# Performance work log

Measured on AMD Instinct MI355X. Metric: run time of the kernel, lower is better.

Reference implementation:

```python
import jax, jax.numpy as jnp
import numpy as np

H = 512  # hidden_dim
IN = 4   # input_dim
OUT = 2  # output_dim
T_OBS = 30
T_PRED = 60
B = 4096


def _gru_cell(x, h, Wih, Whh, bih, bhh):
    # PyTorch GRU cell math. x: (B, D_in), h: (B, H)
    gi = x @ Wih.T + bih          # (B, 3H)
    gh = h @ Whh.T + bhh          # (B, 3H)
    i_r, i_z, i_n = jnp.split(gi, 3, axis=-1)
    h_r, h_z, h_n = jnp.split(gh, 3, axis=-1)
    r = jax.nn.sigmoid(i_r + h_r)
    z = jax.nn.sigmoid(i_z + h_z)
    n = jnp.tanh(i_n + r * h_n)
    return (1.0 - z) * n + z * h


def _gru_layer(xs, h0, Wih, Whh, bih, bhh):
    # xs: (T, B, D_in) -> outputs (T, B, H), final h (B, H)
    def step(h, x):
        h_new = _gru_cell(x, h, Wih, Whh, bih, bhh)
        return h_new, h_new
    h_last, ys = jax.lax.scan(step, h0, xs)
    return ys, h_last


def setup_inputs() -> dict:
    key = jax.random.key(0)
    ks = jax.random.split(key, 16)
    s = 0.05
    inp = {
        "x": jax.random.normal(ks[0], (B, T_OBS, IN), dtype=jnp.float32),
        # encoder layer 0
        "W_ih0": jax.random.normal(ks[1], (3 * H, IN)) * s,
        "W_hh0": jax.random.normal(ks[2], (3 * H, H)) * s,
        "b_ih0": jax.random.normal(ks[3], (3 * H,)) * s,
        "b_hh0": jax.random.normal(ks[4], (3 * H,)) * s,
        # encoder layer 1
        "W_ih1": jax.random.normal(ks[5], (3 * H, H)) * s,
        "W_hh1": jax.random.normal(ks[6], (3 * H, H)) * s,
        "b_ih1": jax.random.normal(ks[7], (3 * H,)) * s,
        "b_hh1": jax.random.normal(ks[8], (3 * H,)) * s,
        # decoder GRU (input_dim = OUT)
        "W_ihd": jax.random.normal(ks[9], (3 * H, OUT)) * s,
        "W_hhd": jax.random.normal(ks[10], (3 * H, H)) * s,
        "b_ihd": jax.random.normal(ks[11], (3 * H,)) * s,
        "b_hhd": jax.random.normal(ks[12], (3 * H,)) * s,
        # output head
        "W_fc": jax.random.normal(ks[13], (OUT, H)) * s,
        "b_fc": jax.random.normal(ks[14], (OUT,)) * s,
    }
    return inp


def reference(x, W_ih0, W_hh0, b_ih0, b_hh0, W_ih1, W_hh1, b_ih1, b_hh1,
              W_ihd, W_hhd, b_ihd, b_hhd, W_fc, b_fc):
    dtype = x.dtype
    xs = jnp.transpose(x, (1, 0, 2))  # (T, B, IN)
    h0 = jnp.zeros((x.shape[0], H), dtype=dtype)
    # 2-layer encoder GRU (dropout=identity at inference)
    ys0, _ = _gru_layer(xs, h0, W_ih0, W_hh0, b_ih0, b_hh0)
    ys1, h_last = _gru_layer(ys0, h0, W_ih1, W_hh1, b_ih1, b_hh1)
    dec_in0 = x[:, -1, :2]  # (B, 2)

    def dec_step(carry, _):
        h, inp = carry
        h_new = _gru_cell(inp, h, W_ihd, W_hhd, b_ihd, b_hhd)
        pred = h_new @ W_fc.T + b_fc  # (B, 2)
        return (h_new, pred), pred

    (_, _), preds = jax.lax.scan(dec_step, (h_last, dec_in0), None, length=T_PRED)
    return jnp.transpose(preds, (1, 0, 2))  # (B, T_PRED, OUT)
```

## Files before the change

### kernel.cpp

```cpp
#include <hip/hip_runtime.h>
#include <math.h>


#define B_SZ  4096
#define H     512
#define H3    1536
#define TOBS  30
#define TPRED 60

typedef float f32x4 __attribute__((ext_vector_type(4)));
typedef short s16x8 __attribute__((ext_vector_type(8)));
typedef __bf16 bf16x8 __attribute__((ext_vector_type(8)));

__device__ __forceinline__ float b2f(unsigned short u) {
    unsigned v = (unsigned)u << 16; return __builtin_bit_cast(float, v);
}
__device__ __forceinline__ unsigned short f2b(float f) {
    unsigned u = __builtin_bit_cast(unsigned, f);
    return (unsigned short)((u + 0x7FFF + ((u >> 16) & 1)) >> 16);
}

typedef __attribute__((address_space(1))) void gvoid;
typedef __attribute__((address_space(3))) void lvoid;
__device__ __forceinline__ void gl16(const void* g, void* l) {
    __builtin_amdgcn_global_load_lds((gvoid*)g, (lvoid*)l, 16, 0, 0);
}

__device__ __forceinline__ f32x4 mfma_bf16(s16x8 a, s16x8 b, f32x4 c) {
    return __builtin_amdgcn_mfma_f32_16x16x32_bf16(
        __builtin_bit_cast(bf16x8, a), __builtin_bit_cast(bf16x8, b), c, 0, 0, 0);
}

__device__ __forceinline__ float sigmoidf_(float v) { return 1.f / (1.f + expf(-v)); }

template<int NJ, int KTOT>
__device__ __forceinline__ void gemm_core2(
    const unsigned short* __restrict__ A, const unsigned short* __restrict__ W,
    int m0, int n0,
    unsigned short* __restrict__ sA, unsigned short* __restrict__ sB,
    f32x4 (&acc)[4][NJ])
{
    const int tid  = threadIdx.x;
    const int lane = tid & 63;
    const int w    = tid >> 6;
    const int wr = w >> 1, wc = w & 1;
    const int lr = lane & 15;
    const int q  = lane >> 4;
    const int wbase = tid & ~63;
    const int NT = KTOT / 64;
    const int ASZ = 128 * 64, BSZ = NJ * 32 * 64;

    auto stage = [&](int buf, int k0) {
        unsigned short* dA = sA + buf * ASZ;
        unsigned short* dB = sB + buf * BSZ;
#pragma unroll
        for (int s = 0; s < 4; ++s) {
            int i = s * 256 + tid;
            int row = i >> 3, p = i & 7;
            int c = p ^ (row & 7);
            gl16(A + (size_t)(m0 + row) * 1024 + k0 + c * 8, dA + (s * 256 + wbase) * 8);
        }
#pragma unroll
        for (int s = 0; s < NJ; ++s) {
            int i = s * 256 + tid;
            int row = i >> 3, p = i & 7;
            int c = p ^ (row & 7);
            gl16(W + (size_t)(n0 + row) * KTOT + k0 + c * 8, dB + (s * 256 + wbase) * 8);
        }
    };

    stage(0, 0);
    __syncthreads();
#pragma unroll
    for (int ti = 0; ti < NT; ++ti) {
        const int cur = ti & 1;
        if (ti + 1 < NT) stage(cur ^ 1, (ti + 1) * 64);
        const unsigned short* cA = sA + cur * ASZ;
        const unsigned short* cB = sB + cur * BSZ;
#pragma unroll
        for (int kk = 0; kk < 64; kk += 32) {
            int qb = (kk >> 3) + q;
            s16x8 af[4], bf[NJ];
#pragma unroll
            for (int fi = 0; fi < 4; ++fi) {
                int r = wr * 64 + fi * 16 + lr;
                af[fi] = *(const s16x8*)&cA[r * 64 + ((qb ^ (r & 7)) * 8)];
            }
#pragma unroll
            for (int fj = 0; fj < NJ; ++fj) {
                int r = wc * (NJ * 16) + fj * 16 + lr;
                bf[fj] = *(const s16x8*)&cB[r * 64 + ((qb ^ (r & 7)) * 8)];
            }
#pragma unroll
            for (int fi = 0; fi < 4; ++fi)
#pragma unroll
                for (int fj = 0; fj < NJ; ++fj)
                    acc[fi][fj] = mfma_bf16(af[fi], bf[fj], acc[fi][fj]);
        }
        __syncthreads();
    }
}

__global__ __launch_bounds__(256)
void gemm_e0(const unsigned short* __restrict__ A, const unsigned short* __restrict__ W,
             const float* __restrict__ x, int t,
             const float* __restrict__ Wih, const float* __restrict__ bih,
             const float* __restrict__ bhh,
             float* __restrict__ hf, unsigned short* __restrict__ hbout)
{
    int bid = (int)blockIdx.x;
    int swz = (bid & 7) * 64 + (bid >> 3);
    const int tile_n = swz & 15;
    const int n0 = tile_n * 96;
    const int m0 = (swz >> 4) * 128;

    __shared__ unsigned short sA[2 * 128 * 64], sB[2 * 96 * 64];
    f32x4 acc[4][3];
#pragma unroll
    for (int i = 0; i < 4; ++i)
#pragma unroll
        for (int j = 0; j < 3; ++j) acc[i][j] = (f32x4){0.f, 0.f, 0.f, 0.f};

    gemm_core2<3, 512>(A, W, m0, n0, sA, sB, acc);

    const int lane = threadIdx.x & 63;
    const int w    = threadIdx.x >> 6;
    const int wrw = w >> 1, wcw = w & 1;
    const int lr = lane & 15, q = lane >> 4;
    const int u = tile_n * 32 + wcw * 16 + lr;

    float4 wrv = *(const float4*)(Wih + (size_t)u * 4);
    float4 wzv = *(const float4*)(Wih + (size_t)(512 + u) * 4);
    float4 wnv = *(const float4*)(Wih + (size_t)(1024 + u) * 4);
    float br_ = bih[u], bz_ = bih[512 + u], bn_ = bih[1024 + u];
    float cr_ = bhh[u], cz_ = bhh[512 + u], cn_ = bhh[1024 + u];

#pragma unroll
    for (int fi = 0; fi < 4; ++fi) {
#pragma unroll
        for (int j = 0; j < 4; ++j) {
            int row = m0 + wrw * 64 + fi * 16 + q * 4 + j;
            float4 xv = *(const float4*)(x + (size_t)row * 120 + t * 4);
            float gir = br_ + xv.x * wrv.x + xv.y * wrv.y + xv.z * wrv.z + xv.w * wrv.w;
            float giz = bz_ + xv.x * wzv.x + xv.y * wzv.y + xv.z * wzv.z + xv.w * wzv.w;
            float gin = bn_ + xv.x * wnv.x + xv.y * wnv.y + xv.z * wnv.z + xv.w * wnv.w;
            float rr = sigmoidf_(gir + acc[fi][0][j] + cr_);
            float zz = sigmoidf_(giz + acc[fi][1][j] + cz_);
            float nn = tanhf(gin + rr * (acc[fi][2][j] + cn_));
            size_t hidx = (size_t)row * 512 + u;
            float hn = (1.f - zz) * nn + zz * hf[hidx];
            hf[hidx] = hn;
            hbout[(size_t)row * 1024 + u] = f2b(hn);
        }
    }
}

__global__ __launch_bounds__(256)
void gemm_e1(const unsigned short* __restrict__ A, const unsigned short* __restrict__ W,
             const float* __restrict__ bih, const float* __restrict__ bhh,
             float* __restrict__ hf, unsigned short* __restrict__ hbout )
{
    int bid = (int)blockIdx.x;
    int swz = (bid & 7) * 64 + (bid >> 3);
    const int tile_n = swz & 15;
    const int n0 = tile_n * 128;
    const int m0 = (swz >> 4) * 128;

    __shared__ unsigned short sA[2 * 128 * 64], sB[2 * 128 * 64];
    f32x4 acc[4][4];
#pragma unroll
    for (int i = 0; i < 4; ++i)
#pragma unroll
        for (int j = 0; j < 4; ++j) acc[i][j] = (f32x4){0.f, 0.f, 0.f, 0.f};

    gemm_core2<4, 1024>(A, W, m0, n0, sA, sB, acc);

    const int lane = threadIdx.x & 63;
    const int w    = threadIdx.x >> 6;
    const int wrw = w >> 1, wcw = w & 1;
    const int lr = lane & 15, q = lane >> 4;
    const int u = tile_n * 32 + wcw * 16 + lr;

    float br_ = bih[u] + bhh[u];
    float bz_ = bih[512 + u] + bhh[512 + u];
    float bni = bih[1024 + u], bnh = bhh[1024 + u];

#pragma unroll
    for (int fi = 0; fi < 4; ++fi) {
#pragma unroll
        for (int j = 0; j < 4; ++j) {
            int row = m0 + wrw * 64 + fi * 16 + q * 4 + j;
            float rr = sigmoidf_(acc[fi][0][j] + br_);
            float zz = sigmoidf_(acc[fi][1][j] + bz_);
            float nn = tanhf(acc[fi][2][j] + bni + rr * (acc[fi][3][j] + bnh));
            size_t hidx = (size_t)row * 512 + u;
            float hn = (1.f - zz) * nn + zz * hf[hidx];
            hf[hidx] = hn;
            hbout[(size_t)row * 1024 + u] = f2b(hn);
        }
    }
}

__global__ __launch_bounds__(256)
void gemm_d(const unsigned short* __restrict__ A ,
            const unsigned short* __restrict__ W,
            const float* __restrict__ dinbuf, int t,
            const float* __restrict__ Wih, const float* __restrict__ bih,
            const float* __restrict__ bhh, const float* __restrict__ bfc,
            float* __restrict__ hf, unsigned short* __restrict__ hbout ,
            float* __restrict__ out)
{
    int bid = (int)blockIdx.x;
    int swz = (bid & 7) * 64 + (bid >> 3);
    const int tile_n = swz & 15;
    const int n0 = tile_n * 128;
    const int m0 = (swz >> 4) * 128;

    __shared__ unsigned short sA[2 * 128 * 64], sB[2 * 128 * 64];
    f32x4 acc[4][4];
#pragma unroll
    for (int i = 0; i < 4; ++i)
#pragma unroll
        for (int j = 0; j < 4; ++j) acc[i][j] = (f32x4){0.f, 0.f, 0.f, 0.f};

    gemm_core2<4, 512>(A, W, m0, n0, sA, sB, acc);

    const int lane = threadIdx.x & 63;
    const int w    = threadIdx.x >> 6;
    const int wrw = w >> 1, wcw = w & 1;
    const int lr = lane & 15, q = lane >> 4;
    const int u = tile_n * 32 + wcw * 16 + lr;

    float wr0 = Wih[(size_t)u * 2],          wr1 = Wih[(size_t)u * 2 + 1];
    float wz0 = Wih[(size_t)(512 + u) * 2],  wz1 = Wih[(size_t)(512 + u) * 2 + 1];
    float wn0 = Wih[(size_t)(1024 + u) * 2], wn1 = Wih[(size_t)(1024 + u) * 2 + 1];
    float br_ = bih[u], bz_ = bih[512 + u], bn_ = bih[1024 + u];
    float cr_ = bhh[u], cz_ = bhh[512 + u], cn_ = bhh[1024 + u];
    float bfc0 = bfc[0], bfc1 = bfc[1];
    const bool wout = (tile_n == 0) && (wcw == 0) && (lr == 0);

#pragma unroll
    for (int fi = 0; fi < 4; ++fi) {
#pragma unroll
        for (int j = 0; j < 4; ++j) {
            int row = m0 + wrw * 64 + fi * 16 + q * 4 + j;
            float p0 = __shfl(acc[fi][3][j], (lane & 48) | 0) + bfc0;
            float p1 = __shfl(acc[fi][3][j], (lane & 48) | 1) + bfc1;
            float x0, x1;
            if (t == 0) { x0 = dinbuf[row * 2]; x1 = dinbuf[row * 2 + 1]; }
            else        { x0 = p0; x1 = p1; }
            float gir = br_ + x0 * wr0 + x1 * wr1;
            float giz = bz_ + x0 * wz0 + x1 * wz1;
            float gin = bn_ + x0 * wn0 + x1 * wn1;
            float rr = sigmoidf_(gir + acc[fi][0][j] + cr_);
            float zz = sigmoidf_(giz + acc[fi][1][j] + cz_);
            float nn = tanhf(gin + rr * (acc[fi][2][j] + cn_));
            size_t hidx = (size_t)row * 512 + u;
            float hn = (1.f - zz) * nn + zz * hf[hidx];
            hf[hidx] = hn;
            hbout[(size_t)row * 1024 + u] = f2b(hn);
            if (t > 0 && wout) {
                out[(size_t)row * 120 + (t - 1) * 2 + 0] = p0;
                out[(size_t)row * 120 + (t - 1) * 2 + 1] = p1;
            }
        }
    }
}

__global__ __launch_bounds__(64)
void fc_last(const unsigned short* __restrict__ hb ,
             const float* __restrict__ Wfc, const float* __restrict__ bfc,
             float* __restrict__ out)
{
    int row = blockIdx.x, lane = threadIdx.x;
    const unsigned short* hrow = hb + (size_t)row * 1024;
    float a0 = 0.f, a1 = 0.f;
#pragma unroll
    for (int kb = 0; kb < 8; ++kb) {
        int k = kb * 64 + lane;
        float hv = b2f(hrow[k]);
        a0 += hv * Wfc[k];
        a1 += hv * Wfc[512 + k];
    }
#pragma unroll
    for (int m = 32; m; m >>= 1) { a0 += __shfl_xor(a0, m); a1 += __shfl_xor(a1, m); }
    if (lane == 0) {
        out[(size_t)row * 120 + 118] = a0 + bfc[0];
        out[(size_t)row * 120 + 119] = a1 + bfc[1];
    }
}

__global__ void wprep_rzn(const float* __restrict__ s, unsigned short* __restrict__ d)
{
    int i = blockIdx.x * 256 + threadIdx.x;
    int c = i >> 9, k = i & 511;
    int ublock = c / 48, rem = c % 48, g = rem >> 4, uoff = rem & 15;
    int u = ublock * 16 + uoff;
    d[i] = f2b(s[((size_t)(g * 512 + u)) * 512 + k]);
}

__global__ void wprep_e1(const float* __restrict__ Wih1, const float* __restrict__ Whh1,
                         unsigned short* __restrict__ d)
{
    int i = blockIdx.x * 256 + threadIdx.x;
    int c = i >> 10, k = i & 1023;
    int ublock = c >> 6, g = (c >> 4) & 3, uoff = c & 15;
    int u = ublock * 16 + uoff;
    float v;
    if (g == 0)      v = (k < 512) ? Wih1[(size_t)u * 512 + k]          : Whh1[(size_t)u * 512 + (k - 512)];
    else if (g == 1) v = (k < 512) ? Wih1[(size_t)(512 + u) * 512 + k]  : Whh1[(size_t)(512 + u) * 512 + (k - 512)];
    else if (g == 2) v = (k < 512) ? Wih1[(size_t)(1024 + u) * 512 + k] : 0.f;
    else             v = (k < 512) ? 0.f : Whh1[(size_t)(1024 + u) * 512 + (k - 512)];
    d[i] = f2b(v);
}

__global__ void wprep_d(const float* __restrict__ Whhd, const float* __restrict__ Wfc,
                        unsigned short* __restrict__ d)
{
    int i = blockIdx.x * 256 + threadIdx.x;
    int c = i >> 9, k = i & 511;
    int ublock = c >> 6, g = (c >> 4) & 3, uoff = c & 15;
    int u = ublock * 16 + uoff;
    float v;
    if (g < 3)           v = Whhd[((size_t)(g * 512 + u)) * 512 + k];
    else if (uoff < 2)   v = Wfc[(size_t)uoff * 512 + k];
    else                 v = 0.f;
    d[i] = f2b(v);
}

__global__ void init_all(const float* __restrict__ x,
                         float* __restrict__ hf0, float* __restrict__ hf1,
                         unsigned short* __restrict__ hbU, unsigned short* __restrict__ hbV,
                         float* __restrict__ dinbuf)
{
    int idx = blockIdx.x * 256 + threadIdx.x;
    if (idx < B_SZ * 512) { hf0[idx] = 0.f; hf1[idx] = 0.f; }
    hbU[idx] = 0; hbV[idx] = 0;
    if (idx < B_SZ * 2)
        dinbuf[idx] = x[(size_t)(idx >> 1) * 120 + 29 * 4 + (idx & 1)];
}

extern "C" void kernel_launch(void* const* d_in, const int* in_sizes, int n_in,
                              void* d_out, int out_size, void* d_ws, size_t ws_size,
                              hipStream_t stream)
{
    const float* x    = (const float*)d_in[0];
    const float* Wih0 = (const float*)d_in[1];
    const float* Whh0 = (const float*)d_in[2];
    const float* bih0 = (const float*)d_in[3];
    const float* bhh0 = (const float*)d_in[4];
    const float* Wih1 = (const float*)d_in[5];
    const float* Whh1 = (const float*)d_in[6];
    const float* bih1 = (const float*)d_in[7];
    const float* bhh1 = (const float*)d_in[8];
    const float* Wihd = (const float*)d_in[9];
    const float* Whhd = (const float*)d_in[10];
    const float* bihd = (const float*)d_in[11];
    const float* bhhd = (const float*)d_in[12];
    const float* Wfc  = (const float*)d_in[13];
    const float* bfc  = (const float*)d_in[14];
    float* out = (float*)d_out;

    char* p = (char*)d_ws;
    float* hf0 = (float*)p;  p += (size_t)B_SZ * 512 * 4;
    float* hf1 = (float*)p;  p += (size_t)B_SZ * 512 * 4;
    unsigned short* hbU = (unsigned short*)p; p += (size_t)B_SZ * 1024 * 2;
    unsigned short* hbV = (unsigned short*)p; p += (size_t)B_SZ * 1024 * 2;
    float* dinbuf = (float*)p; p += (size_t)B_SZ * 2 * 4;
    unsigned short* W0p = (unsigned short*)p; p += (size_t)1536 * 512 * 2;
    unsigned short* W1p = (unsigned short*)p; p += (size_t)2048 * 1024 * 2;
    unsigned short* Wdp = (unsigned short*)p;

    wprep_rzn<<<(1536 * 512) / 256, 256, 0, stream>>>(Whh0, W0p);
    wprep_e1<<<(2048 * 1024) / 256, 256, 0, stream>>>(Wih1, Whh1, W1p);
    wprep_d<<<(2048 * 512) / 256, 256, 0, stream>>>(Whhd, Wfc, Wdp);
    init_all<<<(B_SZ * 1024) / 256, 256, 0, stream>>>(x, hf0, hf1, hbU, hbV, dinbuf);

    unsigned short* hbt[2] = {hbU, hbV};
    for (int t = 0; t < TOBS; ++t) {
        unsigned short* bufR = hbt[t & 1];
        unsigned short* bufW = hbt[(t & 1) ^ 1];
        gemm_e0<<<512, 256, 0, stream>>>(bufR, W0p, x, t, Wih0, bih0, bhh0, hf0, bufW);
        gemm_e1<<<512, 256, 0, stream>>>(bufW, W1p, bih1, bhh1, hf1, bufR + 512);
    }
    for (int t = 0; t < TPRED; ++t) {
        unsigned short* dR = hbt[(t & 1) ^ 1] + 512;
        unsigned short* dW = hbt[t & 1] + 512;
        gemm_d<<<512, 256, 0, stream>>>(dR, Wdp, dinbuf, t, Wihd, bihd, bhhd, bfc,
                                        hf1, dW, out);
    }
    fc_last<<<B_SZ, 64, 0, stream>>>(hbt[1] + 512, Wfc, bfc, out);
}
```

Baseline: 2.499 ms.

## Wavefront-fuse encoder layers into one launch and shrink layer-1 weight padding

Merges the two encoder GRU layers into a single kernel that runs layer 0 at step t alongside layer 1 at step t-1 with 1024 blocks, halving the number of encoder launches and raising per-launch parallelism. Layer-1 weights are repacked from 4 padded gate groups to 3 groups, and the n-gate input and hidden parts go to separate accumulators by K half, which removes a quarter of the layer-1 MFMA work and weight traffic. Hidden-state buffers are split into separate 512-wide ping-pong arrays per layer. The cost is extra register pressure in the unified kernel and a more intricate buffer-indexing scheme.

```diff
diff --git a/kernel.cpp b/kernel.cpp
--- a/kernel.cpp
+++ b/kernel.cpp
@@ -4,7 +4,6 @@
 
 #define B_SZ  4096
 #define H     512
-#define H3    1536
 #define TOBS  30
 #define TPRED 60
 
@@ -33,12 +32,13 @@
 
 __device__ __forceinline__ float sigmoidf_(float v) { return 1.f / (1.f + expf(-v)); }
 
-template<int NJ, int KTOT>
+template<int NJ, int KTOT, int SPLIT>
 __device__ __forceinline__ void gemm_core2(
-    const unsigned short* __restrict__ A, const unsigned short* __restrict__ W,
+    const unsigned short* __restrict__ A0, const unsigned short* __restrict__ A1,
+    const unsigned short* __restrict__ W,
     int m0, int n0,
     unsigned short* __restrict__ sA, unsigned short* __restrict__ sB,
-    f32x4 (&acc)[4][NJ])
+    f32x4 (&acc)[4][NJ + SPLIT])
 {
     const int tid  = threadIdx.x;
     const int lane = tid & 63;
@@ -53,12 +53,14 @@
     auto stage = [&](int buf, int k0) {
         unsigned short* dA = sA + buf * ASZ;
         unsigned short* dB = sB + buf * BSZ;
+        const unsigned short* Ab = (SPLIT && k0 >= 512) ? A1 : A0;
+        const int ak0 = (SPLIT && k0 >= 512) ? k0 - 512 : k0;
 #pragma unroll
         for (int s = 0; s < 4; ++s) {
             int i = s * 256 + tid;
             int row = i >> 3, p = i & 7;
             int c = p ^ (row & 7);
-            gl16(A + (size_t)(m0 + row) * 1024 + k0 + c * 8, dA + (s * 256 + wbase) * 8);
+            gl16(Ab + (size_t)(m0 + row) * 512 + ak0 + c * 8, dA + (s * 256 + wbase) * 8);
         }
 #pragma unroll
         for (int s = 0; s < NJ; ++s) {
@@ -94,34 +96,38 @@
 #pragma unroll
             for (int fi = 0; fi < 4; ++fi)
 #pragma unroll
-                for (int fj = 0; fj < NJ; ++fj)
-                    acc[fi][fj] = mfma_bf16(af[fi], bf[fj], acc[fi][fj]);
+                for (int fj = 0; fj < NJ; ++fj) {
+                    const int dst = (SPLIT && fj == NJ - 1 && ti >= NT / 2) ? NJ : fj;
+                    acc[fi][dst] = mfma_bf16(af[fi], bf[fj], acc[fi][dst]);
+                }
         }
         __syncthreads();
     }
 }
 
 __global__ __launch_bounds__(256)
-void gemm_e0(const unsigned short* __restrict__ A, const unsigned short* __restrict__ W,
-             const float* __restrict__ x, int t,
-             const float* __restrict__ Wih, const float* __restrict__ bih,
-             const float* __restrict__ bhh,
-             float* __restrict__ hf, unsigned short* __restrict__ hbout)
-{
+void gemm_enc(const unsigned short* __restrict__ e1_h0, const unsigned short* __restrict__ e1_h1in,
+              unsigned short* __restrict__ e1_h1out, const unsigned short* __restrict__ W1,
+              const float* __restrict__ bih1, const float* __restrict__ bhh1,
+              float* __restrict__ hf1,
+              const unsigned short* __restrict__ e0_h0in, unsigned short* __restrict__ e0_h0out,
+              const unsigned short* __restrict__ W0,
+              const float* __restrict__ x, int t,
+              const float* __restrict__ Wih0, const float* __restrict__ bih0,
+              const float* __restrict__ bhh0, float* __restrict__ hf0,
+              int roles)
+{
+    __shared__ unsigned short sA[2 * 128 * 64], sB[2 * 96 * 64];
+
     int bid = (int)blockIdx.x;
+    bool isE1;
+    if (roles == 3) { isE1 = bid < 512; bid &= 511; }
+    else            { isE1 = (roles == 1); }
+
     int swz = (bid & 7) * 64 + (bid >> 3);
     const int tile_n = swz & 15;
     const int n0 = tile_n * 96;
     const int m0 = (swz >> 4) * 128;
-
-    __shared__ unsigned short sA[2 * 128 * 64], sB[2 * 96 * 64];
-    f32x4 acc[4][3];
-#pragma unroll
-    for (int i = 0; i < 4; ++i)
-#pragma unroll
-        for (int j = 0; j < 3; ++j) acc[i][j] = (f32x4){0.f, 0.f, 0.f, 0.f};
-
-    gemm_core2<3, 512>(A, W, m0, n0, sA, sB, acc);
 
     const int lane = threadIdx.x & 63;
     const int w    = threadIdx.x >> 6;
@@ -129,74 +135,63 @@
     const int lr = lane & 15, q = lane >> 4;
     const int u = tile_n * 32 + wcw * 16 + lr;
 
-    float4 wrv = *(const float4*)(Wih + (size_t)u * 4);
-    float4 wzv = *(const float4*)(Wih + (size_t)(512 + u) * 4);
-    float4 wnv = *(const float4*)(Wih + (size_t)(1024 + u) * 4);
-    float br_ = bih[u], bz_ = bih[512 + u], bn_ = bih[1024 + u];
-    float cr_ = bhh[u], cz_ = bhh[512 + u], cn_ = bhh[1024 + u];
-
-#pragma unroll
-    for (int fi = 0; fi < 4; ++fi) {
-#pragma unroll
-        for (int j = 0; j < 4; ++j) {
-            int row = m0 + wrw * 64 + fi * 16 + q * 4 + j;
-            float4 xv = *(const float4*)(x + (size_t)row * 120 + t * 4);
-            float gir = br_ + xv.x * wrv.x + xv.y * wrv.y + xv.z * wrv.z + xv.w * wrv.w;
-            float giz = bz_ + xv.x * wzv.x + xv.y * wzv.y + xv.z * wzv.z + xv.w * wzv.w;
-            float gin = bn_ + xv.x * wnv.x + xv.y * wnv.y + xv.z * wnv.z + xv.w * wnv.w;
-            float rr = sigmoidf_(gir + acc[fi][0][j] + cr_);
-            float zz = sigmoidf_(giz + acc[fi][1][j] + cz_);
-            float nn = tanhf(gin + rr * (acc[fi][2][j] + cn_));
-            size_t hidx = (size_t)row * 512 + u;
-            float hn = (1.f - zz) * nn + zz * hf[hidx];
-            hf[hidx] = hn;
-            hbout[(size_t)row * 1024 + u] = f2b(hn);
-        }
-    }
-}
-
-__global__ __launch_bounds__(256)
-void gemm_e1(const unsigned short* __restrict__ A, const unsigned short* __restrict__ W,
-             const float* __restrict__ bih, const float* __restrict__ bhh,
-             float* __restrict__ hf, unsigned short* __restrict__ hbout )
-{
-    int bid = (int)blockIdx.x;
-    int swz = (bid & 7) * 64 + (bid >> 3);
-    const int tile_n = swz & 15;
-    const int n0 = tile_n * 128;
-    const int m0 = (swz >> 4) * 128;
-
-    __shared__ unsigned short sA[2 * 128 * 64], sB[2 * 128 * 64];
-    f32x4 acc[4][4];
-#pragma unroll
-    for (int i = 0; i < 4; ++i)
-#pragma unroll
-        for (int j = 0; j < 4; ++j) acc[i][j] = (f32x4){0.f, 0.f, 0.f, 0.f};
-
-    gemm_core2<4, 1024>(A, W, m0, n0, sA, sB, acc);
-
-    const int lane = threadIdx.x & 63;
-    const int w    = threadIdx.x >> 6;
-    const int wrw = w >> 1, wcw = w & 1;
-    const int lr = lane & 15, q = lane >> 4;
-    const int u = tile_n * 32 + wcw * 16 + lr;
-
-    float br_ = bih[u] + bhh[u];
-    float bz_ = bih[512 + u] + bhh[512 + u];
-    float bni = bih[1024 + u], bnh = bhh[1024 + u];
-
-#pragma unroll
-    for (int fi = 0; fi < 4; ++fi) {
-#pragma unroll
-        for (int j = 0; j < 4; ++j) {
-            int row = m0 + wrw * 64 + fi * 16 + q * 4 + j;
-            float rr = sigmoidf_(acc[fi][0][j] + br_);
-            float zz = sigmoidf_(acc[fi][1][j] + bz_);
-            float nn = tanhf(acc[fi][2][j] + bni + rr * (acc[fi][3][j] + bnh));
-            size_t hidx = (size_t)row * 512 + u;
-            float hn = (1.f - zz) * nn + zz * hf[hidx];
-            hf[hidx] = hn;
-            hbout[(size_t)row * 1024 + u] = f2b(hn);
+    if (isE1) {
+        f32x4 acc[4][4];
+#pragma unroll
+        for (int i = 0; i < 4; ++i)
+#pragma unroll
+            for (int j = 0; j < 4; ++j) acc[i][j] = (f32x4){0.f, 0.f, 0.f, 0.f};
+
+        gemm_core2<3, 1024, 1>(e1_h0, e1_h1in, W1, m0, n0, sA, sB, acc);
+
+        float br_ = bih1[u] + bhh1[u];
+        float bz_ = bih1[512 + u] + bhh1[512 + u];
+        float bni = bih1[1024 + u], bnh = bhh1[1024 + u];
+#pragma unroll
+        for (int fi = 0; fi < 4; ++fi) {
+#pragma unroll
+            for (int j = 0; j < 4; ++j) {
+                int row = m0 + wrw * 64 + fi * 16 + q * 4 + j;
+                float rr = sigmoidf_(acc[fi][0][j] + br_);
+                float zz = sigmoidf_(acc[fi][1][j] + bz_);
+                float nn = tanhf(acc[fi][2][j] + bni + rr * (acc[fi][3][j] + bnh));
+                size_t hidx = (size_t)row * 512 + u;
+                float hn = (1.f - zz) * nn + zz * hf1[hidx];
+                hf1[hidx] = hn;
+                e1_h1out[hidx] = f2b(hn);
+            }
+        }
+    } else {
+        f32x4 acc[4][3];
+#pragma unroll
+        for (int i = 0; i < 4; ++i)
+#pragma unroll
+            for (int j = 0; j < 3; ++j) acc[i][j] = (f32x4){0.f, 0.f, 0.f, 0.f};
+
+        gemm_core2<3, 512, 0>(e0_h0in, e0_h0in, W0, m0, n0, sA, sB, acc);
+
+        float4 wrv = *(const float4*)(Wih0 + (size_t)u * 4);
+        float4 wzv = *(const float4*)(Wih0 + (size_t)(512 + u) * 4);
+        float4 wnv = *(const float4*)(Wih0 + (size_t)(1024 + u) * 4);
+        float br_ = bih0[u], bz_ = bih0[512 + u], bn_ = bih0[1024 + u];
+        float cr_ = bhh0[u], cz_ = bhh0[512 + u], cn_ = bhh0[1024 + u];
+#pragma unroll
+        for (int fi = 0; fi < 4; ++fi) {
+#pragma unroll
+            for (int j = 0; j < 4; ++j) {
+                int row = m0 + wrw * 64 + fi * 16 + q * 4 + j;
+                float4 xv = *(const float4*)(x + (size_t)row * 120 + t * 4);
+                float gir = br_ + xv.x * wrv.x + xv.y * wrv.y + xv.z * wrv.z + xv.w * wrv.w;
+                float giz = bz_ + xv.x * wzv.x + xv.y * wzv.y + xv.z * wzv.z + xv.w * wzv.w;
+                float gin = bn_ + xv.x * wnv.x + xv.y * wnv.y + xv.z * wnv.z + xv.w * wnv.w;
+                float rr = sigmoidf_(gir + acc[fi][0][j] + cr_);
+                float zz = sigmoidf_(giz + acc[fi][1][j] + cz_);
+                float nn = tanhf(gin + rr * (acc[fi][2][j] + cn_));
+                size_t hidx = (size_t)row * 512 + u;
+                float hn = (1.f - zz) * nn + zz * hf0[hidx];
+                hf0[hidx] = hn;
+                e0_h0out[hidx] = f2b(hn);
+            }
         }
     }
 }
@@ -207,7 +202,7 @@
             const float* __restrict__ dinbuf, int t,
             const float* __restrict__ Wih, const float* __restrict__ bih,
             const float* __restrict__ bhh, const float* __restrict__ bfc,
-            float* __restrict__ hf, unsigned short* __restrict__ hbout ,
+            float* __restrict__ hf, unsigned short* __restrict__ hbout,
             float* __restrict__ out)
 {
     int bid = (int)blockIdx.x;
@@ -223,7 +218,7 @@
 #pragma unroll
         for (int j = 0; j < 4; ++j) acc[i][j] = (f32x4){0.f, 0.f, 0.f, 0.f};
 
-    gemm_core2<4, 512>(A, W, m0, n0, sA, sB, acc);
+    gemm_core2<4, 512, 0>(A, A, W, m0, n0, sA, sB, acc);
 
     const int lane = threadIdx.x & 63;
     const int w    = threadIdx.x >> 6;
@@ -258,7 +253,7 @@
             size_t hidx = (size_t)row * 512 + u;
             float hn = (1.f - zz) * nn + zz * hf[hidx];
             hf[hidx] = hn;
-            hbout[(size_t)row * 1024 + u] = f2b(hn);
+            hbout[hidx] = f2b(hn);
             if (t > 0 && wout) {
                 out[(size_t)row * 120 + (t - 1) * 2 + 0] = p0;
                 out[(size_t)row * 120 + (t - 1) * 2 + 1] = p1;
@@ -268,12 +263,11 @@
 }
 
 __global__ __launch_bounds__(64)
-void fc_last(const unsigned short* __restrict__ hb ,
-             const float* __restrict__ Wfc, const float* __restrict__ bfc,
-             float* __restrict__ out)
+void fc_last(const unsigned short* __restrict__ hb, const float* __restrict__ Wfc,
+             const float* __restrict__ bfc, float* __restrict__ out)
 {
     int row = blockIdx.x, lane = threadIdx.x;
-    const unsigned short* hrow = hb + (size_t)row * 1024;
+    const unsigned short* hrow = hb + (size_t)row * 512;
     float a0 = 0.f, a1 = 0.f;
 #pragma unroll
     for (int kb = 0; kb < 8; ++kb) {
@@ -304,13 +298,10 @@
 {
     int i = blockIdx.x * 256 + threadIdx.x;
     int c = i >> 10, k = i & 1023;
-    int ublock = c >> 6, g = (c >> 4) & 3, uoff = c & 15;
+    int ublock = c / 48, rem = c % 48, g = rem >> 4, uoff = rem & 15;
     int u = ublock * 16 + uoff;
-    float v;
-    if (g == 0)      v = (k < 512) ? Wih1[(size_t)u * 512 + k]          : Whh1[(size_t)u * 512 + (k - 512)];
-    else if (g == 1) v = (k < 512) ? Wih1[(size_t)(512 + u) * 512 + k]  : Whh1[(size_t)(512 + u) * 512 + (k - 512)];
-    else if (g == 2) v = (k < 512) ? Wih1[(size_t)(1024 + u) * 512 + k] : 0.f;
-    else             v = (k < 512) ? 0.f : Whh1[(size_t)(1024 + u) * 512 + (k - 512)];
+    float v = (k < 512) ? Wih1[(size_t)(g * 512 + u) * 512 + k]
+                        : Whh1[(size_t)(g * 512 + u) * 512 + (k - 512)];
     d[i] = f2b(v);
 }
 
@@ -330,12 +321,12 @@
 
 __global__ void init_all(const float* __restrict__ x,
                          float* __restrict__ hf0, float* __restrict__ hf1,
-                         unsigned short* __restrict__ hbU, unsigned short* __restrict__ hbV,
+                         unsigned short* __restrict__ h0a, unsigned short* __restrict__ h1a,
                          float* __restrict__ dinbuf)
 {
     int idx = blockIdx.x * 256 + threadIdx.x;
-    if (idx < B_SZ * 512) { hf0[idx] = 0.f; hf1[idx] = 0.f; }
-    hbU[idx] = 0; hbV[idx] = 0;
+    hf0[idx] = 0.f; hf1[idx] = 0.f;
+    h0a[idx] = 0; h1a[idx] = 0;
     if (idx < B_SZ * 2)
         dinbuf[idx] = x[(size_t)(idx >> 1) * 120 + 29 * 4 + (idx & 1)];
 }
@@ -364,30 +355,42 @@
     char* p = (char*)d_ws;
     float* hf0 = (float*)p;  p += (size_t)B_SZ * 512 * 4;
     float* hf1 = (float*)p;  p += (size_t)B_SZ * 512 * 4;
-    unsigned short* hbU = (unsigned short*)p; p += (size_t)B_SZ * 1024 * 2;
-    unsigned short* hbV = (unsigned short*)p; p += (size_t)B_SZ * 1024 * 2;
+    unsigned short* h0b_[2], *h1b_[2];
+    h0b_[0] = (unsigned short*)p; p += (size_t)B_SZ * 512 * 2;
+    h0b_[1] = (unsigned short*)p; p += (size_t)B_SZ * 512 * 2;
+    h1b_[0] = (unsigned short*)p; p += (size_t)B_SZ * 512 * 2;
+    h1b_[1] = (unsigned short*)p; p += (size_t)B_SZ * 512 * 2;
     float* dinbuf = (float*)p; p += (size_t)B_SZ * 2 * 4;
-    unsigned short* W0p = (unsigned short*)p; p += (size_t)1536 * 512 * 2;
-    unsigned short* W1p = (unsigned short*)p; p += (size_t)2048 * 1024 * 2;
-    unsigned short* Wdp = (unsigned short*)p;
+    unsigned short* W0p  = (unsigned short*)p; p += (size_t)1536 * 512 * 2;
+    unsigned short* W1pp = (unsigned short*)p; p += (size_t)1536 * 1024 * 2;
+    unsigned short* Wdp  = (unsigned short*)p;
 
     wprep_rzn<<<(1536 * 512) / 256, 256, 0, stream>>>(Whh0, W0p);
-    wprep_e1<<<(2048 * 1024) / 256, 256, 0, stream>>>(Wih1, Whh1, W1p);
+    wprep_e1<<<(1536 * 1024) / 256, 256, 0, stream>>>(Wih1, Whh1, W1pp);
     wprep_d<<<(2048 * 512) / 256, 256, 0, stream>>>(Whhd, Wfc, Wdp);
-    init_all<<<(B_SZ * 1024) / 256, 256, 0, stream>>>(x, hf0, hf1, hbU, hbV, dinbuf);
-
-    unsigned short* hbt[2] = {hbU, hbV};
-    for (int t = 0; t < TOBS; ++t) {
-        unsigned short* bufR = hbt[t & 1];
-        unsigned short* bufW = hbt[(t & 1) ^ 1];
-        gemm_e0<<<512, 256, 0, stream>>>(bufR, W0p, x, t, Wih0, bih0, bhh0, hf0, bufW);
-        gemm_e1<<<512, 256, 0, stream>>>(bufW, W1p, bih1, bhh1, hf1, bufR + 512);
+    init_all<<<(B_SZ * 512) / 256, 256, 0, stream>>>(x, hf0, hf1, h0b_[0], h1b_[0], dinbuf);
+
+    gemm_enc<<<512, 256, 0, stream>>>(nullptr, nullptr, nullptr, nullptr, nullptr, nullptr,
+                                      nullptr,
+                                      h0b_[0], h0b_[1], W0p, x, 0, Wih0, bih0, bhh0, hf0,
+                                      2);
+    for (int t = 1; t < TOBS; ++t) {
+        int s = t - 1;
+        gemm_enc<<<1024, 256, 0, stream>>>(
+            h0b_[(s + 1) & 1], h1b_[s & 1], h1b_[(s + 1) & 1], W1pp, bih1, bhh1, hf1,
+            h0b_[t & 1], h0b_[(t + 1) & 1], W0p, x, t, Wih0, bih0, bhh0, hf0,
+            3);
+    }
+    {
+        int s = TOBS - 1;
+        gemm_enc<<<512, 256, 0, stream>>>(
+            h0b_[(s + 1) & 1], h1b_[s & 1], h1b_[(s + 1) & 1], W1pp, bih1, bhh1, hf1,
+            nullptr, nullptr, nullptr, nullptr, 0, nullptr, nullptr, nullptr, nullptr,
+            1);
     }
     for (int t = 0; t < TPRED; ++t) {
-        unsigned short* dR = hbt[(t & 1) ^ 1] + 512;
-        unsigned short* dW = hbt[t & 1] + 512;
-        gemm_d<<<512, 256, 0, stream>>>(dR, Wdp, dinbuf, t, Wihd, bihd, bhhd, bfc,
-                                        hf1, dW, out);
-    }
-    fc_last<<<B_SZ, 64, 0, stream>>>(hbt[1] + 512, Wfc, bfc, out);
-}
+        gemm_d<<<512, 256, 0, stream>>>(h1b_[t & 1], Wdp, dinbuf, t, Wihd, bihd, bhhd, bfc,
+                                        hf1, h1b_[(t + 1) & 1], out);
+    }
+    fc_last<<<B_SZ, 64, 0, stream>>>(h1b_[0], Wfc, bfc, out);
+}
```

Result: faster. 2.430 ms (-2.8%).
